# Performance work log

Hardware: AMD Instinct MI355X
Metric: run time of the kernel (lower is better)

Reference implementation:

```python
import jax, jax.numpy as jnp
import numpy as np

DIM = 1024
D_STATE = 16
D_CONV = 4
EXPAND = 2
D_INNER = DIM * EXPAND
DT_RANK = 64  # ceil(1024/16)
N_EXP = 8
TOP_K = 2
HID = DIM * 2
B, T = 2, 2048
EPS = 1e-5


def setup_inputs() -> dict:
    key = jax.random.key(0)
    ks = jax.random.split(key, 16)
    s = 0.02
    # dt bias init (softplus-inverse of dt in [1e-3, 1e-1]) as in the torch code
    dt_init = jnp.exp(jax.random.uniform(ks[0], (D_INNER,)) * (np.log(0.1) - np.log(0.001)) + np.log(0.001))
    dt_proj_b = dt_init + jnp.log(-jnp.expm1(-dt_init))
    A_log = jnp.broadcast_to(jnp.log(jnp.arange(1, D_STATE + 1, dtype=jnp.float32))[None, :], (D_INNER, D_STATE))
    return {
        "x": jax.random.normal(ks[1], (B, T, DIM), jnp.float32),
        "ssm_state": jnp.zeros((B, D_INNER, D_STATE), jnp.float32),
        "conv_state": jnp.zeros((B, D_INNER, D_CONV - 1), jnp.float32),
        "ln1_s": jnp.ones((DIM,), jnp.float32), "ln1_b": jnp.zeros((DIM,), jnp.float32),
        "ln2_s": jnp.ones((DIM,), jnp.float32), "ln2_b": jnp.zeros((DIM,), jnp.float32),
        "in_proj_w": jax.random.normal(ks[2], (2 * D_INNER, DIM), jnp.float32) * s,
        "conv_w": jax.random.normal(ks[3], (D_INNER, 1, D_CONV), jnp.float32) * 0.2,
        "conv_b": jnp.zeros((D_INNER,), jnp.float32),
        "x_proj_w": jax.random.normal(ks[4], (DT_RANK + 2 * D_STATE, D_INNER), jnp.float32) * s,
        "dt_proj_w": jax.random.normal(ks[5], (D_INNER, DT_RANK), jnp.float32) * s,
        "dt_proj_b": dt_proj_b,
        "A_log": A_log,
        "Dp": jnp.ones((D_INNER,), jnp.float32),
        "out_proj_w": jax.random.normal(ks[6], (DIM, D_INNER), jnp.float32) * s,
        "router_w": jax.random.normal(ks[7], (N_EXP, DIM), jnp.float32) * s,
        "w_gate": jax.random.normal(ks[8], (N_EXP, HID, DIM), jnp.float32) * s,
        "w_up": jax.random.normal(ks[9], (N_EXP, HID, DIM), jnp.float32) * s,
        "w_down": jax.random.normal(ks[10], (N_EXP, DIM, HID), jnp.float32) * s,
    }


def _layernorm(x, scale, bias):
    mu = x.mean(-1, keepdims=True)
    var = ((x - mu) ** 2).mean(-1, keepdims=True)
    return (x - mu) * jax.lax.rsqrt(var + EPS) * scale + bias


def _mamba(xn, ssm_state, conv_state, in_proj_w, conv_w, conv_b, x_proj_w, dt_proj_w, dt_proj_b, A_log, Dp, out_proj_w):
    xz = jnp.einsum("btd,ed->bte", xn, in_proj_w)          # [B,T,2*di]
    x_in, z = xz[..., :D_INNER], xz[..., D_INNER:]
    # causal depthwise conv with running buffer
    xc = jnp.concatenate([conv_state, x_in.transpose(0, 2, 1)], axis=2)  # [B,di,T+dc-1]
    new_conv_state = xc[:, :, -(D_CONV - 1):]
    conv = jax.lax.conv_general_dilated(xc, conv_w, (1,), "VALID",
                                        dimension_numbers=("NCH", "OIH", "NCH"),
                                        feature_group_count=D_INNER)
    conv = conv + conv_b[None, :, None]
    xcs = jax.nn.silu(conv).transpose(0, 2, 1)              # [B,T,di]
    proj = jnp.einsum("bti,pi->btp", xcs, x_proj_w)
    dt_raw = proj[..., :DT_RANK]
    Bp = proj[..., DT_RANK:DT_RANK + D_STATE]
    Cp = proj[..., DT_RANK + D_STATE:]
    dt = jax.nn.softplus(jnp.einsum("btr,ir->bti", dt_raw, dt_proj_w) + dt_proj_b)
    A = -jnp.exp(A_log)                                     # [di,ds]

    def step(h, inp):
        dt_t, B_t, C_t, x_t = inp                           # [B,di],[B,ds],[B,ds],[B,di]
        dA = jnp.exp(dt_t[..., None] * A)                   # [B,di,ds]
        dB = dt_t[..., None] * B_t[:, None, :]
        h = dA * h + dB * x_t[..., None]
        y = jnp.sum(h * C_t[:, None, :], -1) + Dp * x_t
        return h, y

    xs = (dt.transpose(1, 0, 2), Bp.transpose(1, 0, 2), Cp.transpose(1, 0, 2), xcs.transpose(1, 0, 2))
    h, ys = jax.lax.scan(step, ssm_state, xs)
    y = ys.transpose(1, 0, 2) * jax.nn.silu(z)
    out = jnp.einsum("bti,di->btd", y, out_proj_w)
    return out, h, new_conv_state


def _moe(x, router_w, w_gate, w_up, w_down):
    Bb, Tt, D = x.shape
    xf = x.reshape(-1, D)                                   # [N,D]
    probs = jax.nn.softmax(xf @ router_w.T, axis=-1)        # [N,E]
    tw, ti = jax.lax.top_k(probs, TOP_K)
    tw = tw / tw.sum(-1, keepdims=True)
    gate = jax.nn.silu(jnp.einsum("nd,ehd->neh", xf, w_gate))
    up = jnp.einsum("nd,ehd->neh", xf, w_up)
    eo = jnp.einsum("neh,edh->ned", gate * up, w_down)      # [N,E,D]
    sel = jnp.take_along_axis(eo, ti[:, :, None], axis=1)   # [N,K,D]
    out = (tw[..., None] * sel).sum(1)
    return out.reshape(Bb, Tt, D)


def reference(x, ssm_state, conv_state, ln1_s, ln1_b, ln2_s, ln2_b, in_proj_w, conv_w, conv_b,
              x_proj_w, dt_proj_w, dt_proj_b, A_log, Dp, out_proj_w, router_w, w_gate, w_up, w_down):
    mamba_out, h, new_conv = _mamba(_layernorm(x, ln1_s, ln1_b), ssm_state, conv_state,
                                    in_proj_w, conv_w, conv_b, x_proj_w, dt_proj_w, dt_proj_b,
                                    A_log, Dp, out_proj_w)
    x1 = x + mamba_out
    out = x1 + _moe(_layernorm(x1, ln2_s, ln2_b), router_w, w_gate, w_up, w_down)
    return out
```

## Files before the change

### kernel.cpp

```cpp
#include <hip/hip_runtime.h>
#include <hip/hip_bf16.h>
#include <math.h>

#define DIM 1024
#define D_STATE 16
#define D_CONV 4
#define D_INNER 2048
#define DT_RANK 64
#define N_EXP 8
#define TOP_K 2
#define HID 2048
#define BB 2
#define TT 2048
#define NTOK (BB*TT)
#define NSLOT (NTOK*TOP_K)
#define EPS 1e-5f
#define NCHUNK 64
#define CLEN (TT/NCHUNK)
#define XPJ_KS 8
#define XPJ_KLEN (D_INNER/XPJ_KS)

#define OFF_R0   ((size_t)0)
#define OFF_R1   ((size_t)4194304)
#define OFF_R2   ((size_t)8388608)
#define OFF_XZ   ((size_t)10485760)
#define OFF_H    OFF_XZ
#define OFF_WU   ((size_t)18874368)
#define OFF_XCS  ((size_t)27262976)
#define OFF_DTP  ((size_t)35651584)
#define OFF_X1   ((size_t)44040192)
#define OFF_PROJ ((size_t)48234496)
#define OFF_TW   ((size_t)48627712)
#define OFF_INT  ((size_t)48635904)
#define OFF_XPW  ((size_t)48668672)
#define IO_TI    0
#define IO_CNT   8192
#define IO_CUR   8200
#define IO_OFS   8208
#define IO_TOK   8216
#define IO_SLOT  16408

typedef __attribute__((ext_vector_type(4))) float f32x4;
typedef __attribute__((ext_vector_type(8))) __bf16 bf16x8;
typedef __attribute__((ext_vector_type(4))) __bf16 bf16x4;

__device__ __forceinline__ float siluf(float v){ return v / (1.f + expf(-v)); }

__device__ __forceinline__ f32x4 mfma16(bf16x8 a, bf16x8 b, f32x4 c){
    return __builtin_amdgcn_mfma_f32_16x16x32_bf16(a, b, c, 0, 0, 0);
}

__device__ __forceinline__ void gload16(const void* g, void* l){
    __builtin_amdgcn_global_load_lds(
        (const __attribute__((address_space(1))) unsigned int*)g,
        (__attribute__((address_space(3))) unsigned int*)l, 16, 0, 0);
}

__device__ __forceinline__ void cvt_store16(__bf16* dst, f32x4 a0, f32x4 a1, f32x4 a2, f32x4 a3){
    bf16x8 p0, p1;
    #pragma unroll
    for (int j = 0; j < 4; ++j){
        p0[j]   = (__bf16)a0[j];
        p0[j+4] = (__bf16)a1[j];
        p1[j]   = (__bf16)a2[j];
        p1[j+4] = (__bf16)a3[j];
    }
    *(bf16x8*)dst = p0;
    *(bf16x8*)(dst+8) = p1;
}

__global__ __launch_bounds__(256) void cvt_w_kernel(const float* __restrict__ src,
    __bf16* __restrict__ dst, int n4)
{
    int i = blockIdx.x*256 + threadIdx.x;
    int stride = gridDim.x*256;
    for (; i < n4; i += stride){
        f32x4 v = *(const f32x4*)(src + (size_t)i*4);
        bf16x4 o;
        o[0] = (__bf16)v[0]; o[1] = (__bf16)v[1];
        o[2] = (__bf16)v[2]; o[3] = (__bf16)v[3];
        *(bf16x4*)(dst + (size_t)i*4) = o;
    }
}

__global__ __launch_bounds__(256) void cvt_w3_kernel(
    const float* __restrict__ s0, __bf16* __restrict__ d0,
    const float* __restrict__ s1, __bf16* __restrict__ d1,
    const float* __restrict__ s2, __bf16* __restrict__ d2, int n4each)
{
    int stride = gridDim.x*256;
    for (int i = blockIdx.x*256 + threadIdx.x; i < n4each; i += stride){
        f32x4 v = *(const f32x4*)(s0 + (size_t)i*4);
        bf16x4 o;
        o[0]=(__bf16)v[0]; o[1]=(__bf16)v[1]; o[2]=(__bf16)v[2]; o[3]=(__bf16)v[3];
        *(bf16x4*)(d0 + (size_t)i*4) = o;
    }
    for (int i = blockIdx.x*256 + threadIdx.x; i < n4each; i += stride){
        f32x4 v = *(const f32x4*)(s1 + (size_t)i*4);
        bf16x4 o;
        o[0]=(__bf16)v[0]; o[1]=(__bf16)v[1]; o[2]=(__bf16)v[2]; o[3]=(__bf16)v[3];
        *(bf16x4*)(d1 + (size_t)i*4) = o;
    }
    for (int i = blockIdx.x*256 + threadIdx.x; i < n4each; i += stride){
        f32x4 v = *(const f32x4*)(s2 + (size_t)i*4);
        bf16x4 o;
        o[0]=(__bf16)v[0]; o[1]=(__bf16)v[1]; o[2]=(__bf16)v[2]; o[3]=(__bf16)v[3];
        *(bf16x4*)(d2 + (size_t)i*4) = o;
    }
}

__global__ __launch_bounds__(256) void cvt_pad_xproj(const float* __restrict__ src,
    __bf16* __restrict__ dst)
{
    int i = blockIdx.x*256 + threadIdx.x;
    int base = i*4;
    int row = base >> 11;
    bf16x4 o;
    if (row < 96){
        f32x4 v = *(const f32x4*)(src + base);
        o[0] = (__bf16)v[0]; o[1] = (__bf16)v[1];
        o[2] = (__bf16)v[2]; o[3] = (__bf16)v[3];
    } else {
        o[0] = (__bf16)0.f; o[1] = (__bf16)0.f;
        o[2] = (__bf16)0.f; o[3] = (__bf16)0.f;
    }
    *(bf16x4*)(dst + base) = o;
}

__global__ __launch_bounds__(256) void ln_kernel(const float* __restrict__ x,
    const float* __restrict__ s, const float* __restrict__ b,
    __bf16* __restrict__ obf)
{
    int t = blockIdx.x;
    const float* xp = x + (size_t)t * DIM;
    float v[4]; float sum = 0.f, sq = 0.f;
    #pragma unroll
    for (int j = 0; j < 4; ++j){
        v[j] = xp[threadIdx.x + 256*j];
        sum += v[j]; sq += v[j]*v[j];
    }
    #pragma unroll
    for (int off = 32; off; off >>= 1){
        sum += __shfl_xor(sum, off, 64);
        sq  += __shfl_xor(sq , off, 64);
    }
    __shared__ float red[4][2];
    int w = threadIdx.x >> 6, lane = threadIdx.x & 63;
    if (lane == 0){ red[w][0] = sum; red[w][1] = sq; }
    __syncthreads();
    sum = red[0][0]+red[1][0]+red[2][0]+red[3][0];
    sq  = red[0][1]+red[1][1]+red[2][1]+red[3][1];
    float mu = sum * (1.f/DIM);
    float var = sq * (1.f/DIM) - mu*mu;
    float r = rsqrtf(var + EPS);
    #pragma unroll
    for (int j = 0; j < 4; ++j){
        int d = threadIdx.x + 256*j;
        obf[(size_t)t*DIM + d] = (__bf16)((v[j]-mu)*r*s[d] + b[d]);
    }
}

__global__ __launch_bounds__(256) void ln2_router_kernel(const float* __restrict__ x,
    const float* __restrict__ s, const float* __restrict__ b,
    const float* __restrict__ rw, __bf16* __restrict__ obf,
    float* __restrict__ tw, int* __restrict__ ti, int* __restrict__ counts)
{
    int t = blockIdx.x;
    const float* xp = x + (size_t)t * DIM;
    float v[4]; float sum = 0.f, sq = 0.f;
    #pragma unroll
    for (int j = 0; j < 4; ++j){
        v[j] = xp[threadIdx.x + 256*j];
        sum += v[j]; sq += v[j]*v[j];
    }
    #pragma unroll
    for (int off = 32; off; off >>= 1){
        sum += __shfl_xor(sum, off, 64);
        sq  += __shfl_xor(sq , off, 64);
    }
    __shared__ float red[4][2];
    __shared__ float red2[4][N_EXP];
    int w = threadIdx.x >> 6, lane = threadIdx.x & 63;
    if (lane == 0){ red[w][0] = sum; red[w][1] = sq; }
    __syncthreads();
    sum = red[0][0]+red[1][0]+red[2][0]+red[3][0];
    sq  = red[0][1]+red[1][1]+red[2][1]+red[3][1];
    float mu = sum * (1.f/DIM);
    float var = sq * (1.f/DIM) - mu*mu;
    float r = rsqrtf(var + EPS);
    float p[N_EXP] = {};
    #pragma unroll
    for (int j = 0; j < 4; ++j){
        int d = threadIdx.x + 256*j;
        float o = (v[j]-mu)*r*s[d] + b[d];
        obf[(size_t)t*DIM + d] = (__bf16)o;
        #pragma unroll
        for (int e = 0; e < N_EXP; ++e) p[e] += o * rw[e*DIM + d];
    }
    #pragma unroll
    for (int e = 0; e < N_EXP; ++e){
        #pragma unroll
        for (int off = 32; off; off >>= 1) p[e] += __shfl_xor(p[e], off, 64);
    }
    if (lane == 0){
        #pragma unroll
        for (int e = 0; e < N_EXP; ++e) red2[w][e] = p[e];
    }
    __syncthreads();
    if (threadIdx.x == 0){
        float q[N_EXP];
        #pragma unroll
        for (int e = 0; e < N_EXP; ++e)
            q[e] = red2[0][e]+red2[1][e]+red2[2][e]+red2[3][e];
        float mx = q[0];
        #pragma unroll
        for (int e = 1; e < N_EXP; ++e) mx = fmaxf(mx, q[e]);
        float ssum = 0.f;
        #pragma unroll
        for (int e = 0; e < N_EXP; ++e){ q[e] = expf(q[e]-mx); ssum += q[e]; }
        int i0 = 0;
        #pragma unroll
        for (int e = 1; e < N_EXP; ++e) if (q[e] > q[i0]) i0 = e;
        int i1 = (i0 == 0) ? 1 : 0;
        #pragma unroll
        for (int e = 0; e < N_EXP; ++e) if (e != i0 && q[e] > q[i1]) i1 = e;
        float w0 = q[i0]/ssum, w1 = q[i1]/ssum;
        float sw = w0 + w1; w0 /= sw; w1 /= sw;
        tw[t*2] = w0; tw[t*2+1] = w1;
        ti[t*2] = i0; ti[t*2+1] = i1;
        atomicAdd(&counts[i0], 1);
        atomicAdd(&counts[i1], 1);
    }
}

template<int MODE, int EPI, int CBF, int SWZ>
__global__ __launch_bounds__(256,3) void mfma_gemm_fast(
    const __bf16* __restrict__ A, const __bf16* __restrict__ W,
    const void* __restrict__ RG, void* __restrict__ Cv,
    const int* __restrict__ tok_of_slot, const int* __restrict__ counts,
    const int* __restrict__ offs, int M, int N, int K, int lda)
{
    int bx = blockIdx.x, by = blockIdx.y;
    if (SWZ){
        int nwg = gridDim.x*gridDim.y;
        int id = by*gridDim.x + bx;
        int swz = (id & 7)*(nwg >> 3) + (id >> 3);
        bx = swz % gridDim.x; by = swz / gridDim.x;
    }
    int e    = (MODE == 0) ? 0 : blockIdx.z;
    int cnt  = (MODE == 0) ? M : counts[e];
    int base = (MODE == 0) ? 0 : offs[e];
    int m0 = by * 128;
    if (m0 >= cnt) return;
    int n0 = bx * 128;
    const __bf16* We = W + (size_t)e * N * K;

    __shared__ __bf16 As[3*128*32];
    __shared__ __bf16 Ws[3*128*32];

    int tid = threadIdx.x;
    int wave = tid >> 6, lane = tid & 63;
    int c0 = wave*2, c1 = wave*2 + 1;
    int lr0 = c0*16 + (lane >> 2);
    int lr1 = c1*16 + (lane >> 2);
    int koff = (((lane & 3) ^ ((lane >> 3) & 3)) * 8);

    int ar0, ar1;
    {
        int m0c = m0 + lr0, m1c = m0 + lr1;
        if (MODE != 0){
            if (m0c >= cnt) m0c = cnt - 1;
            if (m1c >= cnt) m1c = cnt - 1;
        }
        if (MODE == 1){ ar0 = tok_of_slot[base + m0c]; ar1 = tok_of_slot[base + m1c]; }
        else if (MODE == 2){ ar0 = base + m0c; ar1 = base + m1c; }
        else { ar0 = m0c; ar1 = m1c; }
    }
    const __bf16* aS0 = A + (size_t)ar0 * lda + koff;
    const __bf16* aS1 = A + (size_t)ar1 * lda + koff;
    const __bf16* wS0 = We + (size_t)(n0 + lr0) * K + koff;
    const __bf16* wS1 = We + (size_t)(n0 + lr1) * K + koff;
    __bf16* ldsA0 = As + c0*512;
    __bf16* ldsA1 = As + c1*512;
    __bf16* ldsW0 = Ws + c0*512;
    __bf16* ldsW1 = Ws + c1*512;

    int wm = (wave >> 1) * 64, wn = (wave & 1) * 64;
    int fr = lane & 15;
    const int scb = (((lane >> 4) ^ ((lane >> 1) & 3)) * 8);

    f32x4 acc[4][4];
    #pragma unroll
    for (int i = 0; i < 4; ++i)
        #pragma unroll
        for (int j = 0; j < 4; ++j)
            acc[i][j] = (f32x4){0.f, 0.f, 0.f, 0.f};

    int NK = K >> 5;
    gload16(aS0, ldsA0);        gload16(aS1, ldsA1);
    gload16(wS0, ldsW0);        gload16(wS1, ldsW1);
    if (NK > 1){
        gload16(aS0 + 32, ldsA0 + 4096); gload16(aS1 + 32, ldsA1 + 4096);
        gload16(wS0 + 32, ldsW0 + 4096); gload16(wS1 + 32, ldsW1 + 4096);
    }

    int cur = 0;
    for (int t = 0; t < NK; ++t){
        if (t + 2 < NK){
            int nb = cur + 2; if (nb >= 3) nb -= 3;
            int off = nb*4096;
            size_t ko = (size_t)(t+2)*32;
            gload16(aS0 + ko, ldsA0 + off);
            gload16(aS1 + ko, ldsA1 + off);
            gload16(wS0 + ko, ldsW0 + off);
            gload16(wS1 + ko, ldsW1 + off);
            asm volatile("s_waitcnt vmcnt(8)" ::: "memory");
        } else if (t + 1 < NK){
            asm volatile("s_waitcnt vmcnt(4)" ::: "memory");
        } else {
            asm volatile("s_waitcnt vmcnt(0)" ::: "memory");
        }
        __builtin_amdgcn_s_barrier();
        int bo = cur*4096;
        bf16x8 af[4], bf[4];
        #pragma unroll
        for (int i = 0; i < 4; ++i)
            af[i] = *(const bf16x8*)&As[bo + (wm + i*16 + fr)*32 + scb];
        #pragma unroll
        for (int j = 0; j < 4; ++j)
            bf[j] = *(const bf16x8*)&Ws[bo + (wn + j*16 + fr)*32 + scb];
        __builtin_amdgcn_s_setprio(1);
        #pragma unroll
        for (int i = 0; i < 4; ++i)
            #pragma unroll
            for (int j = 0; j < 4; ++j)
                acc[i][j] = mfma16(af[i], bf[j], acc[i][j]);
        __builtin_amdgcn_s_setprio(0);
        __builtin_amdgcn_s_barrier();
        cur = cur + 1; if (cur >= 3) cur -= 3;
    }

    int orow = (lane >> 4) * 4;
    int ocol = lane & 15;
    #pragma unroll
    for (int i = 0; i < 4; ++i){
        #pragma unroll
        for (int jj = 0; jj < 4; ++jj){
            #pragma unroll
            for (int j = 0; j < 4; ++j){
                int m = m0 + wm + i*16 + orow + j;
                int n = n0 + wn + jj*16 + ocol;
                if (m < cnt){
                    size_t row = (size_t)(base + m);
                    float v = acc[i][jj][j];
                    if (EPI == 1) v += ((const float*)RG)[row * (size_t)N + n];
                    if (CBF) ((__bf16*)Cv)[row * (size_t)N + n] = (__bf16)v;
                    else     ((float* )Cv)[row * (size_t)N + n] = v;
                }
            }
        }
    }
}

__global__ __launch_bounds__(256,3) void moe_gateup_fast(
    const __bf16* __restrict__ A, const __bf16* __restrict__ Wg,
    const __bf16* __restrict__ Wu, const int* __restrict__ tok_of_slot,
    const int* __restrict__ counts, const int* __restrict__ offs,
    __bf16* __restrict__ H)
{
    int e = blockIdx.z;
    int cnt = counts[e];
    int base = offs[e];
    int n0 = blockIdx.x * 128;
    const __bf16* Wge = Wg + (size_t)e * HID * DIM;
    const __bf16* Wue = Wu + (size_t)e * HID * DIM;

    __shared__ __bf16 As[2*64*32];
    __shared__ __bf16 Gs[2*128*32];
    __shared__ __bf16 Us[2*128*32];

    int tid = threadIdx.x;
    int wave = tid >> 6, lane = tid & 63;
    int lrow = lane >> 2;
    int koff = (((lane & 3) ^ ((lane >> 3) & 3)) * 8);

    const __bf16* gS0 = Wge + (size_t)(n0 + wave*32      + lrow) * DIM + koff;
    const __bf16* gS1 = Wge + (size_t)(n0 + wave*32 + 16 + lrow) * DIM + koff;
    const __bf16* uS0 = Wue + (size_t)(n0 + wave*32      + lrow) * DIM + koff;
    const __bf16* uS1 = Wue + (size_t)(n0 + wave*32 + 16 + lrow) * DIM + koff;
    __bf16* ldsA  = As + wave*512;
    __bf16* ldsG0 = Gs + (wave*2    )*512;
    __bf16* ldsG1 = Gs + (wave*2 + 1)*512;
    __bf16* ldsU0 = Us + (wave*2    )*512;
    __bf16* ldsU1 = Us + (wave*2 + 1)*512;

    int fr = lane & 15;
    const int scb = (((lane >> 4) ^ ((lane >> 1) & 3)) * 8);
    int orow = (lane >> 4) * 4;
    int ocol = lane & 15;
    const int NK = DIM >> 5;

    for (int mb = blockIdx.y; mb * 64 < cnt; mb += gridDim.y){
        int m0 = mb * 64;
        int mc = m0 + wave*16 + lrow;
        if (mc >= cnt) mc = cnt - 1;
        const __bf16* aS = A + (size_t)tok_of_slot[base + mc] * DIM + koff;

        f32x4 accg[4][2], accu[4][2];
        #pragma unroll
        for (int i = 0; i < 4; ++i)
            #pragma unroll
            for (int j = 0; j < 2; ++j){
                accg[i][j] = (f32x4){0.f, 0.f, 0.f, 0.f};
                accu[i][j] = (f32x4){0.f, 0.f, 0.f, 0.f};
            }

        gload16(aS, ldsA);
        gload16(gS0, ldsG0); gload16(gS1, ldsG1);
        gload16(uS0, ldsU0); gload16(uS1, ldsU1);

        int bo = 0;
        for (int t = 0; t < NK; ++t){
            if (t + 1 < NK){
                int nA = (bo ^ 1) * 2048, nW = (bo ^ 1) * 4096;
                size_t ko = (size_t)(t+1)*32;
                gload16(aS + ko, ldsA + nA);
                gload16(gS0 + ko, ldsG0 + nW); gload16(gS1 + ko, ldsG1 + nW);
                gload16(uS0 + ko, ldsU0 + nW); gload16(uS1 + ko, ldsU1 + nW);
                asm volatile("s_waitcnt vmcnt(5)" ::: "memory");
            } else {
                asm volatile("s_waitcnt vmcnt(0)" ::: "memory");
            }
            __builtin_amdgcn_s_barrier();
            int boA = bo*2048, boW = bo*4096;
            bf16x8 af[4], gf[2], uf[2];
            #pragma unroll
            for (int i = 0; i < 4; ++i)
                af[i] = *(const bf16x8*)&As[boA + (i*16 + fr)*32 + scb];
            #pragma unroll
            for (int j = 0; j < 2; ++j){
                gf[j] = *(const bf16x8*)&Gs[boW + (wave*32 + j*16 + fr)*32 + scb];
                uf[j] = *(const bf16x8*)&Us[boW + (wave*32 + j*16 + fr)*32 + scb];
            }
            __builtin_amdgcn_s_setprio(1);
            #pragma unroll
            for (int i = 0; i < 4; ++i)
                #pragma unroll
                for (int j = 0; j < 2; ++j){
                    accg[i][j] = mfma16(af[i], gf[j], accg[i][j]);
                    accu[i][j] = mfma16(af[i], uf[j], accu[i][j]);
                }
            __builtin_amdgcn_s_setprio(0);
            __builtin_amdgcn_s_barrier();
            bo ^= 1;
        }

        #pragma unroll
        for (int i = 0; i < 4; ++i){
            #pragma unroll
            for (int j = 0; j < 2; ++j){
                #pragma unroll
                for (int j4 = 0; j4 < 4; ++j4){
                    int m = m0 + i*16 + orow + j4;
                    if (m < cnt){
                        size_t row = (size_t)(base + m);
                        int n = n0 + wave*32 + j*16 + ocol;
                        float g = accg[i][j][j4], u = accu[i][j][j4];
                        H[row * (size_t)HID + n] = (__bf16)(siluf(g) * u);
                    }
                }
            }
        }
    }
}

__global__ __launch_bounds__(256,3) void xproj_ks_kernel(
    const __bf16* __restrict__ A, const __bf16* __restrict__ W,
    float* __restrict__ Cpart)
{
    int m0 = blockIdx.y * 128;
    int kbeg = blockIdx.z * XPJ_KLEN;

    __shared__ __bf16 As[3*128*32];
    __shared__ __bf16 Ws[3*128*32];

    int tid = threadIdx.x;
    int wave = tid >> 6, lane = tid & 63;
    int c0 = wave*2, c1 = wave*2 + 1;
    int lr0 = c0*16 + (lane >> 2);
    int lr1 = c1*16 + (lane >> 2);
    int koff = (((lane & 3) ^ ((lane >> 3) & 3)) * 8);

    const __bf16* aS0 = A + (size_t)(m0 + lr0) * D_INNER + kbeg + koff;
    const __bf16* aS1 = A + (size_t)(m0 + lr1) * D_INNER + kbeg + koff;
    const __bf16* wS0 = W + (size_t)lr0 * D_INNER + kbeg + koff;
    const __bf16* wS1 = W + (size_t)lr1 * D_INNER + kbeg + koff;
    __bf16* ldsA0 = As + c0*512;
    __bf16* ldsA1 = As + c1*512;
    __bf16* ldsW0 = Ws + c0*512;
    __bf16* ldsW1 = Ws + c1*512;

    int wm = (wave >> 1) * 64, wn = (wave & 1) * 64;
    int fr = lane & 15;
    const int scb = (((lane >> 4) ^ ((lane >> 1) & 3)) * 8);

    f32x4 acc[4][4];
    #pragma unroll
    for (int i = 0; i < 4; ++i)
        #pragma unroll
        for (int j = 0; j < 4; ++j)
            acc[i][j] = (f32x4){0.f, 0.f, 0.f, 0.f};

    gload16(aS0, ldsA0); gload16(aS1, ldsA1);
    gload16(wS0, ldsW0); gload16(wS1, ldsW1);
    gload16(aS0 + 32, ldsA0 + 4096); gload16(aS1 + 32, ldsA1 + 4096);
    gload16(wS0 + 32, ldsW0 + 4096); gload16(wS1 + 32, ldsW1 + 4096);

    const int NK = XPJ_KLEN >> 5;
    int cur = 0;
    for (int t = 0; t < NK; ++t){
        if (t + 2 < NK){
            int nb = cur + 2; if (nb >= 3) nb -= 3;
            int off = nb*4096;
            size_t ko = (size_t)(t+2)*32;
            gload16(aS0 + ko, ldsA0 + off);
            gload16(aS1 + ko, ldsA1 + off);
            gload16(wS0 + ko, ldsW0 + off);
            gload16(wS1 + ko, ldsW1 + off);
            asm volatile("s_waitcnt vmcnt(8)" ::: "memory");
        } else if (t + 1 < NK){
            asm volatile("s_waitcnt vmcnt(4)" ::: "memory");
        } else {
            asm volatile("s_waitcnt vmcnt(0)" ::: "memory");
        }
        __builtin_amdgcn_s_barrier();
        int bo = cur*4096;
        bf16x8 af[4], bf[4];
        #pragma unroll
        for (int i = 0; i < 4; ++i)
            af[i] = *(const bf16x8*)&As[bo + (wm + i*16 + fr)*32 + scb];
        #pragma unroll
        for (int j = 0; j < 4; ++j)
            bf[j] = *(const bf16x8*)&Ws[bo + (wn + j*16 + fr)*32 + scb];
        __builtin_amdgcn_s_setprio(1);
        #pragma unroll
        for (int i = 0; i < 4; ++i)
            #pragma unroll
            for (int j = 0; j < 4; ++j)
                acc[i][j] = mfma16(af[i], bf[j], acc[i][j]);
        __builtin_amdgcn_s_setprio(0);
        __builtin_amdgcn_s_barrier();
        cur = cur + 1; if (cur >= 3) cur -= 3;
    }

    float* Cz = Cpart + (size_t)blockIdx.z * NTOK * 128;
    int orow = (lane >> 4) * 4;
    int ocol = lane & 15;
    #pragma unroll
    for (int i = 0; i < 4; ++i){
        #pragma unroll
        for (int jj = 0; jj < 4; ++jj){
            #pragma unroll
            for (int j = 0; j < 4; ++j){
                int m = m0 + wm + i*16 + orow + j;
                int n = wn + jj*16 + ocol;
                Cz[(size_t)m * 128 + n] = acc[i][jj][j];
            }
        }
    }
}

__global__ __launch_bounds__(256) void xproj_reduce(const float* __restrict__ Cpart,
    float* __restrict__ proj)
{
    int idx = blockIdx.x*256 + threadIdx.x;
    int t = idx / 96, n = idx - t*96;
    float s = 0.f;
    #pragma unroll
    for (int z = 0; z < XPJ_KS; ++z)
        s += Cpart[(size_t)z * NTOK * 128 + (size_t)t * 128 + n];
    proj[idx] = s;
}

__global__ __launch_bounds__(256,2) void dt_gemm(
    const float* __restrict__ A, const float* __restrict__ W,
    const float* __restrict__ bias, float* __restrict__ C,
    int M, int N, int K, int lda)
{
    int m0 = blockIdx.y * 128;
    int n0 = blockIdx.x * 128;

    __shared__ __bf16 As[128*32];
    __shared__ __bf16 Ws[128*32];

    int tid = threadIdx.x;
    int srow = tid >> 1;
    int scol = (tid & 1) * 16;

    const float* af = A + (size_t)(m0 + srow) * lda + scol;
    const float* wptr = W + (size_t)(n0 + srow) * K + scol;

    f32x4 raf[4], rw[4];
    #pragma unroll
    for (int q = 0; q < 4; ++q){
        raf[q] = *(const f32x4*)(af + q*4);
        rw[q]  = *(const f32x4*)(wptr + q*4);
    }

    int wave = tid >> 6, lane = tid & 63;
    int wm = (wave >> 1) * 64, wn = (wave & 1) * 64;
    int fr = lane & 15, fk = (lane >> 4) * 8;

    f32x4 acc[4][4];
    #pragma unroll
    for (int i = 0; i < 4; ++i)
        #pragma unroll
        for (int j = 0; j < 4; ++j)
            acc[i][j] = (f32x4){0.f, 0.f, 0.f, 0.f};

    for (int k0 = 0; k0 < K; k0 += 32){
        cvt_store16(&As[srow*32 + scol], raf[0], raf[1], raf[2], raf[3]);
        cvt_store16(&Ws[srow*32 + scol], rw[0], rw[1], rw[2], rw[3]);
        __syncthreads();
        if (k0 + 32 < K){
            #pragma unroll
            for (int q = 0; q < 4; ++q){
                raf[q] = *(const f32x4*)(af + k0 + 32 + q*4);
                rw[q]  = *(const f32x4*)(wptr + k0 + 32 + q*4);
            }
        }
        bf16x8 afr[4], bfr[4];
        #pragma unroll
        for (int i = 0; i < 4; ++i)
            afr[i] = *(const bf16x8*)&As[(wm + i*16 + fr)*32 + fk];
        #pragma unroll
        for (int i = 0; i < 4; ++i)
            bfr[i] = *(const bf16x8*)&Ws[(wn + i*16 + fr)*32 + fk];
        #pragma unroll
        for (int i = 0; i < 4; ++i)
            #pragma unroll
            for (int j = 0; j < 4; ++j)
                acc[i][j] = mfma16(afr[i], bfr[j], acc[i][j]);
        __syncthreads();
    }

    int orow = (lane >> 4) * 4;
    int ocol = lane & 15;
    #pragma unroll
    for (int i = 0; i < 4; ++i){
        #pragma unroll
        for (int jj = 0; jj < 4; ++jj){
            #pragma unroll
            for (int j = 0; j < 4; ++j){
                int m = m0 + wm + i*16 + orow + j;
                int n = n0 + wn + jj*16 + ocol;
                if (m < M && n < N){
                    float v = acc[i][jj][j] + bias[n];
                    v = (v > 20.f) ? v : log1pf(expf(v));
                    C[(size_t)m * N + n] = v;
                }
            }
        }
    }
}

__global__ __launch_bounds__(256) void conv_kernel(const float* __restrict__ xz,
    const float* __restrict__ cs, const float* __restrict__ cw,
    const float* __restrict__ cb, __bf16* __restrict__ xcs_bf)
{
    int idx = blockIdx.x*256 + threadIdx.x;
    int d = idx & (D_INNER-1);
    int bt = idx >> 11;
    int b = bt >> 11;
    int t = bt & (TT-1);
    float acc = cb[d];
    #pragma unroll
    for (int k = 0; k < 4; ++k){
        int tau = t + k - 3;
        float xv;
        if (tau >= 0) xv = xz[(size_t)(b*TT + tau)*(2*D_INNER) + d];
        else          xv = cs[((size_t)b*D_INNER + d)*3 + (tau + 3)];
        acc += cw[d*4 + k] * xv;
    }
    xcs_bf[idx] = (__bf16)siluf(acc);
}

__global__ __launch_bounds__(256) void scan_pass1(const float* __restrict__ dtp,
    const float* __restrict__ proj, const float* __restrict__ xz,
    const float* __restrict__ cs, const float* __restrict__ cw,
    const float* __restrict__ cb, const float* __restrict__ A_log,
    float* __restrict__ hend, float* __restrict__ sumdt)
{
    int gid = blockIdx.x*256 + threadIdx.x;
    int bd = gid & (BB*D_INNER-1);
    int chunk = gid >> 12;
    int b = bd >> 11, d = bd & (D_INNER-1);
    float As[D_STATE], h[D_STATE];
    #pragma unroll
    for (int s = 0; s < D_STATE; ++s){
        As[s] = -__expf(A_log[d*D_STATE + s]);
        h[s] = 0.f;
    }
    float cw0 = cw[d*4], cw1 = cw[d*4+1], cw2 = cw[d*4+2], cw3 = cw[d*4+3];
    float cbd = cb[d];
    int t0 = chunk*CLEN;
    int base = b*TT + t0;
    float w0, w1, w2;
    if (chunk == 0){
        size_t cbase = ((size_t)b*D_INNER + d)*3;
        w0 = cs[cbase]; w1 = cs[cbase+1]; w2 = cs[cbase+2];
    } else {
        w0 = xz[(size_t)(base-3)*(2*D_INNER) + d];
        w1 = xz[(size_t)(base-2)*(2*D_INNER) + d];
        w2 = xz[(size_t)(base-1)*(2*D_INNER) + d];
    }
    float sdt = 0.f;
    for (int t = 0; t < CLEN; ++t){
        size_t bt = (size_t)(base + t);
        float dt = dtp[bt*D_INNER + d];
        float xv = xz[bt*(2*D_INNER) + d];
        float acc = cbd;
        acc += cw0*w0; acc += cw1*w1; acc += cw2*w2; acc += cw3*xv;
        float x = siluf(acc);
        w0 = w1; w1 = w2; w2 = xv;
        f32x4 Bv[4];
        #pragma unroll
        for (int q = 0; q < 4; ++q) Bv[q] = *(const f32x4*)(proj + bt*96 + DT_RANK + q*4);
        float dtx = dt * x;
        sdt += dt;
        #pragma unroll
        for (int s = 0; s < D_STATE; ++s)
            h[s] = __expf(dt*As[s])*h[s] + Bv[s>>2][s&3]*dtx;
    }
    size_t hb = ((size_t)bd*NCHUNK + chunk)*D_STATE;
    #pragma unroll
    for (int q = 0; q < 4; ++q)
        *(f32x4*)(hend + hb + q*4) = (f32x4){h[q*4], h[q*4+1], h[q*4+2], h[q*4+3]};
    sumdt[bd*NCHUNK + chunk] = sdt;
}

__global__ __launch_bounds__(256) void scan_combine(const float* __restrict__ hend,
    const float* __restrict__ sumdt, const float* __restrict__ A_log,
    const float* __restrict__ ssm0, float* __restrict__ hstart)
{
    int gid = blockIdx.x*256 + threadIdx.x;
    int s = gid & 15;
    int bd = gid >> 4;
    int b = bd >> 11, d = bd & (D_INNER-1);
    float As = -__expf(A_log[d*D_STATE + s]);
    float h = ssm0[((size_t)b*D_INNER + d)*D_STATE + s];
    for (int c = 0; c < NCHUNK; ++c){
        size_t idx = ((size_t)bd*NCHUNK + c)*D_STATE + s;
        hstart[idx] = h;
        h = hend[idx] + __expf(As * sumdt[bd*NCHUNK + c]) * h;
    }
}

__global__ __launch_bounds__(256) void scan_pass3(const float* __restrict__ dtp,
    const float* __restrict__ proj, const float* __restrict__ xz,
    const float* __restrict__ cs, const float* __restrict__ cw,
    const float* __restrict__ cb, const float* __restrict__ A_log,
    const float* __restrict__ Dp, const float* __restrict__ hstart,
    __bf16* __restrict__ ym)
{
    int gid = blockIdx.x*256 + threadIdx.x;
    int bd = gid & (BB*D_INNER-1);
    int chunk = gid >> 12;
    int b = bd >> 11, d = bd & (D_INNER-1);
    float As[D_STATE], h[D_STATE];
    #pragma unroll
    for (int s = 0; s < D_STATE; ++s)
        As[s] = -__expf(A_log[d*D_STATE + s]);
    size_t hb = ((size_t)bd*NCHUNK + chunk)*D_STATE;
    #pragma unroll
    for (int q = 0; q < 4; ++q){
        f32x4 hv = *(const f32x4*)(hstart + hb + q*4);
        h[q*4] = hv[0]; h[q*4+1] = hv[1]; h[q*4+2] = hv[2]; h[q*4+3] = hv[3];
    }
    float Dd = Dp[d];
    float cw0 = cw[d*4], cw1 = cw[d*4+1], cw2 = cw[d*4+2], cw3 = cw[d*4+3];
    float cbd = cb[d];
    int t0 = chunk*CLEN;
    int base = b*TT + t0;
    float w0, w1, w2;
    if (chunk == 0){
        size_t cbase = ((size_t)b*D_INNER + d)*3;
        w0 = cs[cbase]; w1 = cs[cbase+1]; w2 = cs[cbase+2];
    } else {
        w0 = xz[(size_t)(base-3)*(2*D_INNER) + d];
        w1 = xz[(size_t)(base-2)*(2*D_INNER) + d];
        w2 = xz[(size_t)(base-1)*(2*D_INNER) + d];
    }
    for (int t = 0; t < CLEN; ++t){
        size_t bt = (size_t)(base + t);
        float dt = dtp[bt*D_INNER + d];
        float xv = xz[bt*(2*D_INNER) + d];
        float acc = cbd;
        acc += cw0*w0; acc += cw1*w1; acc += cw2*w2; acc += cw3*xv;
        float x = siluf(acc);
        w0 = w1; w1 = w2; w2 = xv;
        f32x4 Bv[4], Cv[4];
        #pragma unroll
        for (int q = 0; q < 4; ++q){
            Bv[q] = *(const f32x4*)(proj + bt*96 + DT_RANK + q*4);
            Cv[q] = *(const f32x4*)(proj + bt*96 + DT_RANK + D_STATE + q*4);
        }
        float dtx = dt * x;
        float p = 0.f;
        #pragma unroll
        for (int s = 0; s < D_STATE; ++s){
            h[s] = __expf(dt*As[s])*h[s] + Bv[s>>2][s&3]*dtx;
            p += h[s] * Cv[s>>2][s&3];
        }
        float y = p + Dd*x;
        float z = xz[bt*(2*D_INNER) + D_INNER + d];
        float sz = z / (1.f + __expf(-z));
        ym[bt*D_INNER + d] = (__bf16)(y * sz);
    }
}

__global__ void offs_kernel(const int* __restrict__ counts, int* __restrict__ offs)
{
    if (threadIdx.x == 0 && blockIdx.x == 0){
        int s = 0;
        for (int e = 0; e < N_EXP; ++e){ offs[e] = s; s += counts[e]; }
    }
}

__global__ __launch_bounds__(256) void assign_kernel(const int* __restrict__ ti,
    const int* __restrict__ offs, int* __restrict__ cursors,
    int* __restrict__ tok_of_slot, int* __restrict__ slot_of)
{
    int t = blockIdx.x*256 + threadIdx.x;
    if (t >= NTOK) return;
    #pragma unroll
    for (int k = 0; k < TOP_K; ++k){
        int e = ti[t*2 + k];
        int pos = atomicAdd(&cursors[e], 1);
        int slot = offs[e] + pos;
        tok_of_slot[slot] = t;
        slot_of[t*2 + k] = slot;
    }
}

__global__ __launch_bounds__(256) void final_kernel(const float* __restrict__ x1,
    const __bf16* __restrict__ down_out, const float* __restrict__ tw,
    const int* __restrict__ slot_of, float* __restrict__ out)
{
    int idx4 = blockIdx.x*256 + threadIdx.x;
    int t = idx4 >> 8;
    int c = idx4 & 255;
    float w0 = tw[t*2], w1 = tw[t*2+1];
    size_t s0 = (size_t)slot_of[t*2] * DIM;
    size_t s1 = (size_t)slot_of[t*2+1] * DIM;
    float4 a = *(const float4*)(x1 + (size_t)t*DIM + c*4);
    bf16x4 d0 = *(const bf16x4*)(down_out + s0 + c*4);
    bf16x4 d1 = *(const bf16x4*)(down_out + s1 + c*4);
    float4 r;
    r.x = a.x + w0*(float)d0[0] + w1*(float)d1[0];
    r.y = a.y + w0*(float)d0[1] + w1*(float)d1[1];
    r.z = a.z + w0*(float)d0[2] + w1*(float)d1[2];
    r.w = a.w + w0*(float)d0[3] + w1*(float)d1[3];
    *(float4*)(out + (size_t)t*DIM + c*4) = r;
}

extern "C" void kernel_launch(void* const* d_in, const int* in_sizes, int n_in,
                              void* d_out, int out_size, void* d_ws, size_t ws_size,
                              hipStream_t stream)
{
    const float* x        = (const float*)d_in[0];
    const float* ssm0     = (const float*)d_in[1];
    const float* conv0    = (const float*)d_in[2];
    const float* ln1_s    = (const float*)d_in[3];
    const float* ln1_b    = (const float*)d_in[4];
    const float* ln2_s    = (const float*)d_in[5];
    const float* ln2_b    = (const float*)d_in[6];
    const float* in_proj  = (const float*)d_in[7];
    const float* conv_w   = (const float*)d_in[8];
    const float* conv_b   = (const float*)d_in[9];
    const float* x_proj   = (const float*)d_in[10];
    const float* dt_proj  = (const float*)d_in[11];
    const float* dt_b     = (const float*)d_in[12];
    const float* A_log    = (const float*)d_in[13];
    const float* Dp       = (const float*)d_in[14];
    const float* out_proj = (const float*)d_in[15];
    const float* router_w = (const float*)d_in[16];
    const float* w_gate   = (const float*)d_in[17];
    const float* w_up     = (const float*)d_in[18];
    const float* w_down   = (const float*)d_in[19];
    float* out = (float*)d_out;

    float* ws = (float*)d_ws;
    __bf16* xn_bf  = (__bf16*)(ws + OFF_R0);
    float*  hend   = ws + OFF_R0;
    __bf16* ym_bf  = (__bf16*)(ws + OFF_R0);
    float*  xpart  = ws + OFF_R1;
    float*  hst    = ws + OFF_R1;
    __bf16* dnout  = (__bf16*)(ws + OFF_R1);
    float*  sdt    = ws + OFF_R2;
    __bf16* opbf   = (__bf16*)(ws + OFF_R2);
    __bf16* xn2bf  = (__bf16*)(ws + OFF_R2);
    float*  xz     = ws + OFF_XZ;
    __bf16* H      = (__bf16*)(ws + OFF_H);
    __bf16* wubf   = (__bf16*)(ws + OFF_WU);
    __bf16* wdbf   = (__bf16*)(ws + OFF_XCS);
    float*  dtp    = ws + OFF_DTP;
    __bf16* ipbf   = (__bf16*)(ws + OFF_DTP);
    __bf16* wgbf   = (__bf16*)(ws + OFF_DTP);
    __bf16* xcs_bf = (__bf16*)(ws + OFF_X1);
    float*  x1     = ws + OFF_X1;
    float*  proj   = ws + OFF_PROJ;
    float*  tw     = ws + OFF_TW;
    __bf16* xpw    = (__bf16*)(ws + OFF_XPW);
    int*    ip     = (int*)(ws + OFF_INT);
    int* ti          = ip + IO_TI;
    int* counts      = ip + IO_CNT;
    int* cursors     = ip + IO_CUR;
    int* offs        = ip + IO_OFS;
    int* tok_of_slot = ip + IO_TOK;
    int* slot_of     = ip + IO_SLOT;

    hipMemsetAsync(counts, 0, 16*sizeof(int), stream);

    cvt_w_kernel<<<1024, 256, 0, stream>>>(in_proj, ipbf, (2*D_INNER*DIM)/4);
    ln_kernel<<<NTOK, 256, 0, stream>>>(x, ln1_s, ln1_b, xn_bf);
    mfma_gemm_fast<0,0,0,1><<<dim3(32,32), 256, 0, stream>>>(xn_bf, ipbf, nullptr, xz,
        nullptr, nullptr, nullptr, NTOK, 2*D_INNER, DIM, DIM);
    conv_kernel<<<(NTOK*D_INNER)/256, 256, 0, stream>>>(xz, conv0, conv_w, conv_b, xcs_bf);
    cvt_pad_xproj<<<256, 256, 0, stream>>>(x_proj, xpw);
    xproj_ks_kernel<<<dim3(1,32,XPJ_KS), 256, 0, stream>>>(xcs_bf, xpw, xpart);
    xproj_reduce<<<(NTOK*96)/256, 256, 0, stream>>>(xpart, proj);
    dt_gemm<<<dim3(16,32), 256, 0, stream>>>(proj, dt_proj, dt_b, dtp,
        NTOK, D_INNER, DT_RANK, 96);
    scan_pass1<<<1024, 256, 0, stream>>>(dtp, proj, xz, conv0, conv_w, conv_b, A_log, hend, sdt);
    scan_combine<<<256, 256, 0, stream>>>(hend, sdt, A_log, ssm0, hst);
    scan_pass3<<<1024, 256, 0, stream>>>(dtp, proj, xz, conv0, conv_w, conv_b, A_log, Dp, hst, ym_bf);
    cvt_w_kernel<<<512, 256, 0, stream>>>(out_proj, opbf, (DIM*D_INNER)/4);
    mfma_gemm_fast<0,1,0,1><<<dim3(8,32), 256, 0, stream>>>(ym_bf, opbf, x, x1,
        nullptr, nullptr, nullptr, NTOK, DIM, D_INNER, D_INNER);
    ln2_router_kernel<<<NTOK, 256, 0, stream>>>(x1, ln2_s, ln2_b, router_w,
        xn2bf, tw, ti, counts);
    offs_kernel<<<1, 64, 0, stream>>>(counts, offs);
    assign_kernel<<<NTOK/256, 256, 0, stream>>>(ti, offs, cursors, tok_of_slot, slot_of);
    cvt_w3_kernel<<<2048, 256, 0, stream>>>(w_gate, wgbf, w_up, wubf, w_down, wdbf,
        (N_EXP*HID*DIM)/4);
    moe_gateup_fast<<<dim3(HID/128, 32, N_EXP), 256, 0, stream>>>(xn2bf, wgbf, wubf,
        tok_of_slot, counts, offs, H);
    mfma_gemm_fast<2,0,1,0><<<dim3(DIM/128, 64, N_EXP), 256, 0, stream>>>(H, wdbf, nullptr, dnout,
        tok_of_slot, counts, offs, NSLOT, DIM, HID, HID);
    final_kernel<<<(NTOK*DIM/4)/256, 256, 0, stream>>>(x1, dnout, tw, slot_of, out);
}
```

Before: 726.3 us.

## Restructure MoE gate/up GEMM into 8-wave 256x128 tiles with phased prefetch

Replaces the 4-wave 64x128 gate/up expert GEMM with an 8-wave kernel computing 256-row by 128-column tiles with K-step 64. Global loads for the next stage are split across four MFMA phases separated by barriers, which overlaps memory traffic with compute in a ping-pong schedule. Larger tiles raise weight reuse per block and cut redundant reloads of gate/up weights. In exchange the kernel uses much more LDS and registers (32 accumulators per thread), the grid shrinks to 4 M-blocks per expert, and there are more barriers per K-step.

```diff
diff --git a/kernel.cpp b/kernel.cpp
--- a/kernel.cpp
+++ b/kernel.cpp
@@ -362,7 +362,7 @@
     }
 }
 
-__global__ __launch_bounds__(256,3) void moe_gateup_fast(
+__global__ __launch_bounds__(512,2) void moe_gateup_8p(
     const __bf16* __restrict__ A, const __bf16* __restrict__ Wg,
     const __bf16* __restrict__ Wu, const int* __restrict__ tok_of_slot,
     const int* __restrict__ counts, const int* __restrict__ offs,
@@ -375,96 +375,173 @@
     const __bf16* Wge = Wg + (size_t)e * HID * DIM;
     const __bf16* Wue = Wu + (size_t)e * HID * DIM;
 
-    __shared__ __bf16 As[2*64*32];
-    __shared__ __bf16 Gs[2*128*32];
-    __shared__ __bf16 Us[2*128*32];
+    __shared__ __bf16 As[2*256*64];
+    __shared__ __bf16 Gs[2*128*64];
+    __shared__ __bf16 Us[2*128*64];
 
     int tid = threadIdx.x;
     int wave = tid >> 6, lane = tid & 63;
-    int lrow = lane >> 2;
-    int koff = (((lane & 3) ^ ((lane >> 3) & 3)) * 8);
-
-    const __bf16* gS0 = Wge + (size_t)(n0 + wave*32      + lrow) * DIM + koff;
-    const __bf16* gS1 = Wge + (size_t)(n0 + wave*32 + 16 + lrow) * DIM + koff;
-    const __bf16* uS0 = Wue + (size_t)(n0 + wave*32      + lrow) * DIM + koff;
-    const __bf16* uS1 = Wue + (size_t)(n0 + wave*32 + 16 + lrow) * DIM + koff;
-    __bf16* ldsA  = As + wave*512;
-    __bf16* ldsG0 = Gs + (wave*2    )*512;
-    __bf16* ldsG1 = Gs + (wave*2 + 1)*512;
-    __bf16* ldsU0 = Us + (wave*2    )*512;
-    __bf16* ldsU1 = Us + (wave*2 + 1)*512;
-
+    int wr = wave >> 1, wc = wave & 1;
     int fr = lane & 15;
-    const int scb = (((lane >> 4) ^ ((lane >> 1) & 3)) * 8);
+    int srow = lane >> 3;
+    int sslot = lane & 7;
+    int sxor = (sslot ^ srow) * 8;
+
+    __bf16* ldsA = As + wave*512 + (size_t)lane*8;
+    __bf16* ldsG = Gs + wave*512 + (size_t)lane*8;
+    __bf16* ldsU = Us + wave*512 + (size_t)lane*8;
+
+    const __bf16* gSrc[2];
+    const __bf16* uSrc[2];
+    #pragma unroll
+    for (int r = 0; r < 2; ++r){
+        int row = n0 + r*64 + wave*8 + srow;
+        gSrc[r] = Wge + (size_t)row * DIM + sxor;
+        uSrc[r] = Wue + (size_t)row * DIM + sxor;
+    }
+
+    const int s0 = (((lane >> 4)    ) ^ (fr & 7)) * 8;
+    const int s1 = (((lane >> 4) + 4) ^ (fr & 7)) * 8;
     int orow = (lane >> 4) * 4;
     int ocol = lane & 15;
-    const int NK = DIM >> 5;
-
-    for (int mb = blockIdx.y; mb * 64 < cnt; mb += gridDim.y){
-        int m0 = mb * 64;
-        int mc = m0 + wave*16 + lrow;
-        if (mc >= cnt) mc = cnt - 1;
-        const __bf16* aS = A + (size_t)tok_of_slot[base + mc] * DIM + koff;
-
-        f32x4 accg[4][2], accu[4][2];
+    const int NKT = DIM / 64;
+
+    for (int mb = blockIdx.y; mb * 256 < cnt; mb += gridDim.y){
+        int m0 = mb * 256;
+        const __bf16* aSrc[4];
+        #pragma unroll
+        for (int r = 0; r < 4; ++r){
+            int m = m0 + r*64 + wave*8 + srow;
+            if (m >= cnt) m = cnt - 1;
+            aSrc[r] = A + (size_t)tok_of_slot[base + m] * DIM + sxor;
+        }
+
+        f32x4 accg[4][4], accu[4][4];
         #pragma unroll
         for (int i = 0; i < 4; ++i)
             #pragma unroll
-            for (int j = 0; j < 2; ++j){
+            for (int j = 0; j < 4; ++j){
                 accg[i][j] = (f32x4){0.f, 0.f, 0.f, 0.f};
                 accu[i][j] = (f32x4){0.f, 0.f, 0.f, 0.f};
             }
 
-        gload16(aS, ldsA);
-        gload16(gS0, ldsG0); gload16(gS1, ldsG1);
-        gload16(uS0, ldsU0); gload16(uS1, ldsU1);
-
-        int bo = 0;
-        for (int t = 0; t < NK; ++t){
-            if (t + 1 < NK){
-                int nA = (bo ^ 1) * 2048, nW = (bo ^ 1) * 4096;
-                size_t ko = (size_t)(t+1)*32;
-                gload16(aS + ko, ldsA + nA);
-                gload16(gS0 + ko, ldsG0 + nW); gload16(gS1 + ko, ldsG1 + nW);
-                gload16(uS0 + ko, ldsU0 + nW); gload16(uS1 + ko, ldsU1 + nW);
-                asm volatile("s_waitcnt vmcnt(5)" ::: "memory");
-            } else {
-                asm volatile("s_waitcnt vmcnt(0)" ::: "memory");
+        #pragma unroll
+        for (int r = 0; r < 4; ++r) gload16(aSrc[r], ldsA + r*4096);
+        #pragma unroll
+        for (int r = 0; r < 2; ++r){
+            gload16(gSrc[r], ldsG + r*4096);
+            gload16(uSrc[r], ldsU + r*4096);
+        }
+        asm volatile("s_waitcnt vmcnt(0)" ::: "memory");
+        __builtin_amdgcn_s_barrier();
+
+        for (int t = 0; t < NKT; ++t){
+            int buf = t & 1;
+            int boA = buf*16384, boGU = buf*8192;
+            int nbA = (buf^1)*16384, nbGU = (buf^1)*8192;
+            size_t ko = (size_t)(t+1)*64;
+            bool pf = (t + 1 < NKT);
+            bf16x8 af[4][2];
+
+            if (pf){
+                gload16(aSrc[0] + ko, ldsA + nbA);
+                gload16(aSrc[1] + ko, ldsA + nbA + 4096);
+                gload16(aSrc[2] + ko, ldsA + nbA + 8192);
+            }
+            #pragma unroll
+            for (int i = 0; i < 4; ++i){
+                af[i][0] = *(const bf16x8*)&As[boA + (wr*64 + i*16 + fr)*64 + s0];
+                af[i][1] = *(const bf16x8*)&As[boA + (wr*64 + i*16 + fr)*64 + s1];
+            }
+            {
+                bf16x8 gf0 = *(const bf16x8*)&Gs[boGU + (wc*64 + 0*16 + fr)*64 + s0];
+                bf16x8 gf1 = *(const bf16x8*)&Gs[boGU + (wc*64 + 0*16 + fr)*64 + s1];
+                bf16x8 uf0 = *(const bf16x8*)&Us[boGU + (wc*64 + 0*16 + fr)*64 + s0];
+                bf16x8 uf1 = *(const bf16x8*)&Us[boGU + (wc*64 + 0*16 + fr)*64 + s1];
+                __builtin_amdgcn_s_setprio(1);
+                #pragma unroll
+                for (int i = 0; i < 4; ++i){
+                    accg[i][0] = mfma16(af[i][0], gf0, accg[i][0]);
+                    accg[i][0] = mfma16(af[i][1], gf1, accg[i][0]);
+                    accu[i][0] = mfma16(af[i][0], uf0, accu[i][0]);
+                    accu[i][0] = mfma16(af[i][1], uf1, accu[i][0]);
+                }
+                __builtin_amdgcn_s_setprio(0);
             }
             __builtin_amdgcn_s_barrier();
-            int boA = bo*2048, boW = bo*4096;
-            bf16x8 af[4], gf[2], uf[2];
-            #pragma unroll
-            for (int i = 0; i < 4; ++i)
-                af[i] = *(const bf16x8*)&As[boA + (i*16 + fr)*32 + scb];
-            #pragma unroll
-            for (int j = 0; j < 2; ++j){
-                gf[j] = *(const bf16x8*)&Gs[boW + (wave*32 + j*16 + fr)*32 + scb];
-                uf[j] = *(const bf16x8*)&Us[boW + (wave*32 + j*16 + fr)*32 + scb];
-            }
-            __builtin_amdgcn_s_setprio(1);
-            #pragma unroll
-            for (int i = 0; i < 4; ++i)
+
+            if (pf){
+                gload16(aSrc[3] + ko, ldsA + nbA + 12288);
+                gload16(gSrc[0] + ko, ldsG + nbGU);
+                gload16(gSrc[1] + ko, ldsG + nbGU + 4096);
+            }
+            {
+                bf16x8 gf0 = *(const bf16x8*)&Gs[boGU + (wc*64 + 1*16 + fr)*64 + s0];
+                bf16x8 gf1 = *(const bf16x8*)&Gs[boGU + (wc*64 + 1*16 + fr)*64 + s1];
+                bf16x8 uf0 = *(const bf16x8*)&Us[boGU + (wc*64 + 1*16 + fr)*64 + s0];
+                bf16x8 uf1 = *(const bf16x8*)&Us[boGU + (wc*64 + 1*16 + fr)*64 + s1];
+                __builtin_amdgcn_s_setprio(1);
                 #pragma unroll
-                for (int j = 0; j < 2; ++j){
-                    accg[i][j] = mfma16(af[i], gf[j], accg[i][j]);
-                    accu[i][j] = mfma16(af[i], uf[j], accu[i][j]);
+                for (int i = 0; i < 4; ++i){
+                    accg[i][1] = mfma16(af[i][0], gf0, accg[i][1]);
+                    accg[i][1] = mfma16(af[i][1], gf1, accg[i][1]);
+                    accu[i][1] = mfma16(af[i][0], uf0, accu[i][1]);
+                    accu[i][1] = mfma16(af[i][1], uf1, accu[i][1]);
                 }
-            __builtin_amdgcn_s_setprio(0);
+                __builtin_amdgcn_s_setprio(0);
+            }
             __builtin_amdgcn_s_barrier();
-            bo ^= 1;
+
+            if (pf){
+                gload16(uSrc[0] + ko, ldsU + nbGU);
+                gload16(uSrc[1] + ko, ldsU + nbGU + 4096);
+            }
+            {
+                bf16x8 gf0 = *(const bf16x8*)&Gs[boGU + (wc*64 + 2*16 + fr)*64 + s0];
+                bf16x8 gf1 = *(const bf16x8*)&Gs[boGU + (wc*64 + 2*16 + fr)*64 + s1];
+                bf16x8 uf0 = *(const bf16x8*)&Us[boGU + (wc*64 + 2*16 + fr)*64 + s0];
+                bf16x8 uf1 = *(const bf16x8*)&Us[boGU + (wc*64 + 2*16 + fr)*64 + s1];
+                __builtin_amdgcn_s_setprio(1);
+                #pragma unroll
+                for (int i = 0; i < 4; ++i){
+                    accg[i][2] = mfma16(af[i][0], gf0, accg[i][2]);
+                    accg[i][2] = mfma16(af[i][1], gf1, accg[i][2]);
+                    accu[i][2] = mfma16(af[i][0], uf0, accu[i][2]);
+                    accu[i][2] = mfma16(af[i][1], uf1, accu[i][2]);
+                }
+                __builtin_amdgcn_s_setprio(0);
+            }
+            __builtin_amdgcn_s_barrier();
+
+            {
+                bf16x8 gf0 = *(const bf16x8*)&Gs[boGU + (wc*64 + 3*16 + fr)*64 + s0];
+                bf16x8 gf1 = *(const bf16x8*)&Gs[boGU + (wc*64 + 3*16 + fr)*64 + s1];
+                bf16x8 uf0 = *(const bf16x8*)&Us[boGU + (wc*64 + 3*16 + fr)*64 + s0];
+                bf16x8 uf1 = *(const bf16x8*)&Us[boGU + (wc*64 + 3*16 + fr)*64 + s1];
+                __builtin_amdgcn_s_setprio(1);
+                #pragma unroll
+                for (int i = 0; i < 4; ++i){
+                    accg[i][3] = mfma16(af[i][0], gf0, accg[i][3]);
+                    accg[i][3] = mfma16(af[i][1], gf1, accg[i][3]);
+                    accu[i][3] = mfma16(af[i][0], uf0, accu[i][3]);
+                    accu[i][3] = mfma16(af[i][1], uf1, accu[i][3]);
+                }
+                __builtin_amdgcn_s_setprio(0);
+            }
+            asm volatile("s_waitcnt vmcnt(0)" ::: "memory");
+            __builtin_amdgcn_s_barrier();
         }
 
         #pragma unroll
         for (int i = 0; i < 4; ++i){
             #pragma unroll
-            for (int j = 0; j < 2; ++j){
+            for (int j = 0; j < 4; ++j){
                 #pragma unroll
                 for (int j4 = 0; j4 < 4; ++j4){
-                    int m = m0 + i*16 + orow + j4;
+                    int m = m0 + wr*64 + i*16 + orow + j4;
                     if (m < cnt){
                         size_t row = (size_t)(base + m);
-                        int n = n0 + wave*32 + j*16 + ocol;
+                        int n = n0 + wc*64 + j*16 + ocol;
                         float g = accg[i][j][j4], u = accu[i][j][j4];
                         H[row * (size_t)HID + n] = (__bf16)(siluf(g) * u);
                     }
@@ -944,7 +1021,7 @@
     assign_kernel<<<NTOK/256, 256, 0, stream>>>(ti, offs, cursors, tok_of_slot, slot_of);
     cvt_w3_kernel<<<2048, 256, 0, stream>>>(w_gate, wgbf, w_up, wubf, w_down, wdbf,
         (N_EXP*HID*DIM)/4);
-    moe_gateup_fast<<<dim3(HID/128, 32, N_EXP), 256, 0, stream>>>(xn2bf, wgbf, wubf,
+    moe_gateup_8p<<<dim3(HID/128, 4, N_EXP), 512, 0, stream>>>(xn2bf, wgbf, wubf,
         tok_of_slot, counts, offs, H);
     mfma_gemm_fast<2,0,1,0><<<dim3(DIM/128, 64, N_EXP), 256, 0, stream>>>(H, wdbf, nullptr, dnout,
         tok_of_slot, counts, offs, NSLOT, DIM, HID, HID);
```

Measured after the change: 769.0 us. 1.06x slower.
